# Kernel optimization log

Hardware: AMD Instinct MI355X
Metric: run time of the kernel (lower is better)

Reference implementation:

```python
import jax, jax.numpy as jnp
import numpy as np
from jax import lax

N, IN_CH, OUT_CH, KERNEL, D = 16, 256, 256, 3, 4096
FACTOR = 2  # upsampling factor
RESAMPLE_K = (1.0, 3.0, 3.0, 1.0)


def _fir_kernel():
    # _setup_kernel: normalize to sum 1; upsample path scales by gain * factor
    k = np.asarray(RESAMPLE_K, dtype=np.float32)
    k = k / k.sum()
    return k * FACTOR  # gain = 1


def setup_inputs() -> dict:
    key = jax.random.key(0)
    k1, k2, k3 = jax.random.split(key, 3)
    x = jax.random.normal(k1, (N, IN_CH, D), dtype=jnp.float32)
    weight = jax.random.normal(k2, (OUT_CH, IN_CH, KERNEL), dtype=jnp.float32) * 0.05
    bias = jax.random.normal(k3, (OUT_CH,), dtype=jnp.float32) * 0.05
    return {"x": x, "weight": weight, "bias": bias}


def _upfirdn1d(x, k, pad0, pad1):
    # up=down=1 path of StyleGAN2 upfirdn1d: pad, then TRUE convolution with FIR k
    # (torch native impl flips k before F.conv1d). Depthwise via [N*C,1,L] reshape.
    n, c, _ = x.shape
    xp = jnp.pad(x, ((0, 0), (0, 0), (pad0, pad1)))
    kr = k[::-1][None, None, :]  # flip -> correlation == convolution
    y = lax.conv_general_dilated(
        xp.reshape(n * c, 1, -1), kr, window_strides=(1,), padding=[(0, 0)],
        dimension_numbers=("NCH", "OIH", "NCH"))
    return y.reshape(n, c, -1)


def _upsample_conv_1d(x, w):
    # torch: w reshaped/flipped/permuted then conv_transpose1d(stride=factor).
    # conv_transpose with that transformed weight == correlation with the ORIGINAL
    # w on an input dilated by `factor` with (convH-1) padding on both sides
    # (output_padding = 0 for these shapes).
    convH = w.shape[2]
    y = lax.conv_general_dilated(
        x, w, window_strides=(1,), padding=[(convH - 1, convH - 1)],
        lhs_dilation=(FACTOR,), dimension_numbers=("NCH", "OIH", "NCH"))
    k = jnp.asarray(_fir_kernel())
    p = k.shape[0] - FACTOR - (convH - 1)  # = 0 here
    pad0 = (p + 1) // 2 + FACTOR - 1
    pad1 = p // 2 + 1
    return _upfirdn1d(y, k, pad0, pad1)  # -> [N, C_out, D * FACTOR]


def reference(x, weight, bias):
    y = _upsample_conv_1d(x, weight)
    return y + bias[None, :, None]
```

## Files before the change

kernel.cpp:

```cpp
#include <hip/hip_runtime.h>
#include <hip/hip_bf16.h>

#define N_   16
#define CI_  256
#define CO_  256
#define D_   4096
#define DO_  8192
#define KTOT 768
#define XTROWS 4098
#define WT_ELEMS (512 * KTOT)
#define XT_ELEMS ((size_t)N_ * XTROWS * 256)

typedef short frag8 __attribute__((ext_vector_type(8)));
typedef float facc4 __attribute__((ext_vector_type(4)));

static __device__ __forceinline__ unsigned short f2bf(float f) {
    union { __hip_bfloat16 h; unsigned short u; } cv;
    cv.h = __float2bfloat16(f);
    return cv.u;
}

static __device__ __forceinline__ unsigned int pack2(float lo, float hi) {
    return (unsigned int)f2bf(lo) | ((unsigned int)f2bf(hi) << 16);
}

static __device__ __forceinline__ void async16(unsigned short* lds, const unsigned short* g) {
    __builtin_amdgcn_global_load_lds(
        (const __attribute__((address_space(1))) unsigned int*)g,
        (__attribute__((address_space(3))) unsigned int*)lds, 16, 0, 0);
}

#define DSR_(dst, addr, litstr) \
    asm volatile("ds_read_b128 %0, %1 offset:" litstr : "=&v"(dst) : "v"(addr))

__global__ __launch_bounds__(256) void prep_wt(const float* __restrict__ w,
                                               unsigned short* __restrict__ Wt) {
    const int ci = threadIdx.x;
    const int co = blockIdx.x;
    const float* wp = w + ((size_t)co * CI_ + ci) * 3;
    const float w0 = wp[0], w1 = wp[1], w2 = wp[2];
    const float e0 = 0.25f * w1 + 0.75f * w0;
    const float e1 = 0.75f * w2 + 0.75f * w1 + 0.25f * w0;
    const float e2 = 0.25f * w2;
    const float o0 = 0.25f * w0;
    const float o1 = 0.25f * w2 + 0.75f * w1 + 0.75f * w0;
    const float o2 = 0.75f * w2 + 0.25f * w1;
    unsigned short* pe = Wt + (size_t)(co * 2 + 0) * KTOT;
    unsigned short* po = Wt + (size_t)(co * 2 + 1) * KTOT;
    pe[0 * 256 + ci] = f2bf(e0); pe[1 * 256 + ci] = f2bf(e1); pe[2 * 256 + ci] = f2bf(e2);
    po[0 * 256 + ci] = f2bf(o0); po[1 * 256 + ci] = f2bf(o1); po[2 * 256 + ci] = f2bf(o2);
}

__global__ __launch_bounds__(256) void prep_xt2(const float* __restrict__ x,
                                                unsigned short* __restrict__ xt) {
    __shared__ unsigned int Lp[32][133];
    const int tid = threadIdx.x;
    const int t0  = blockIdx.x * 32;
    const int n   = blockIdx.y;
    const float* xn = x + (size_t)n * CI_ * D_;
    unsigned short* slab = xt + (size_t)n * XTROWS * 256;

    if (t0 == 0 && tid < 128)       ((unsigned int*)slab)[tid] = 0u;
    if (t0 == D_ - 32 && tid < 128) ((unsigned int*)(slab + (size_t)(XTROWS - 1) * 256))[tid] = 0u;

    const int cp_l  = tid >> 3;
    const int t_off = (tid & 7) * 4;

    #pragma unroll
    for (int p = 0; p < 4; ++p) {
        const int ci0 = p * 64 + cp_l * 2;
        float4 a = *(const float4*)(xn + (size_t)ci0 * D_ + t0 + t_off);
        float4 b = *(const float4*)(xn + (size_t)(ci0 + 1) * D_ + t0 + t_off);
        const int cp = p * 32 + cp_l;
        Lp[t_off + 0][cp] = pack2(a.x, b.x);
        Lp[t_off + 1][cp] = pack2(a.y, b.y);
        Lp[t_off + 2][cp] = pack2(a.z, b.z);
        Lp[t_off + 3][cp] = pack2(a.w, b.w);
    }
    __syncthreads();

    #pragma unroll
    for (int it = 0; it < 4; ++it) {
        const int row = it * 8 + (tid >> 5);
        const int c4  = (tid & 31) * 4;
        uint4 v;
        v.x = Lp[row][c4 + 0];
        v.y = Lp[row][c4 + 1];
        v.z = Lp[row][c4 + 2];
        v.w = Lp[row][c4 + 3];
        *(uint4*)(slab + (size_t)(1 + t0 + row) * 256 + c4 * 2) = v;
    }
}

__global__ __launch_bounds__(512, 2) void gemm_upfir8(
    const unsigned short* __restrict__ Wt, const unsigned short* __restrict__ xt,
    const float* __restrict__ bias, float* __restrict__ out)
{
    __shared__ __align__(16) unsigned short SL[65536];

    const int tid  = threadIdx.x;
    const int lane = tid & 63;
    const int wid  = tid >> 6;
    const int quad = lane >> 4;
    const int l16  = lane & 15;

    const int bt0 = blockIdx.x * 256;
    const int bm0 = blockIdx.y * 256;
    const int n   = blockIdx.z;

    const int srow = wid * 16 + (lane >> 2);
    const int cg   = (lane & 3) ^ ((lane >> 3) & 3);
    const unsigned short* sA = Wt + (size_t)(bm0 + srow) * KTOT + cg * 8;
    const unsigned short* sB = xt + (size_t)n * XTROWS * 256
                                  + (size_t)(bt0 + srow) * 256 + cg * 8;

    #define STAGE_A(u, mh) do {                                                     \
        async16(SL + (((u)&1)*16384 + (mh)*8192 + 0*4096 + wid*512),                \
                sA + (size_t)(mh)*128*KTOT + (u)*64 + 0);                           \
        async16(SL + (((u)&1)*16384 + (mh)*8192 + 1*4096 + wid*512),                \
                sA + (size_t)(mh)*128*KTOT + (u)*64 + 32); } while (0)
    #define STAGE_B(u, th) do {                                                     \
        async16(SL + (32768 + ((u)&1)*16384 + (th)*8192 + 0*4096 + wid*512),        \
                sB + (size_t)(th)*128*256 + (u)*64 + 0);                            \
        async16(SL + (32768 + ((u)&1)*16384 + (th)*8192 + 1*4096 + wid*512),        \
                sB + (size_t)(th)*128*256 + (u)*64 + 32); } while (0)

    const int swz = quad ^ ((l16 >> 1) & 3);
    const int mh  = wid & 1;
    const int wm  = mh * 128;
    const int wt  = ((wid >> 1) & 3) * 64;
    const unsigned base = (unsigned)(size_t)&SL[0];
    const unsigned aB = base + (unsigned)(mh * 16384 + l16 * 64 + swz * 16);
    const unsigned bB = base + 65536u
                      + (unsigned)(((wid >> 2) & 1) * 16384
                                   + (((wid >> 1) & 1) * 64 + l16) * 64 + swz * 16);

    facc4 acc[8][4] = {};

    STAGE_A(0, 0); STAGE_A(0, 1); STAGE_B(0, 0); STAGE_B(0, 1);
    STAGE_A(1, 0); STAGE_A(1, 1);
    asm volatile("s_waitcnt vmcnt(4)" ::: "memory");
    __builtin_amdgcn_s_barrier();

    #define MM(m, t)                                                                 \
        acc[m][t] = __builtin_amdgcn_mfma_f32_16x16x32_bf16(a[m][0], b[t][0], acc[m][t], 0, 0, 0); \
        acc[m][t] = __builtin_amdgcn_mfma_f32_16x16x32_bf16(a[m][1], b[t][1], acc[m][t], 0, 0, 0);

    #pragma unroll 2
    for (int u = 0; u < 12; ++u) {
        const unsigned au = aB + (unsigned)((u & 1) << 15);
        const unsigned bu = bB + (unsigned)((u & 1) << 15);
        frag8 a[8][2], b[4][2];

        DSR_(a[0][0], au, "0");    DSR_(a[0][1], au, "8192");
        DSR_(a[1][0], au, "1024"); DSR_(a[1][1], au, "9216");
        DSR_(a[2][0], au, "2048"); DSR_(a[2][1], au, "10240");
        DSR_(a[3][0], au, "3072"); DSR_(a[3][1], au, "11264");
        DSR_(b[0][0], bu, "0");    DSR_(b[0][1], bu, "8192");
        DSR_(b[1][0], bu, "1024"); DSR_(b[1][1], bu, "9216");
        if (u < 11) STAGE_B(u + 1, 0);
        __builtin_amdgcn_s_barrier();
        asm volatile("s_waitcnt lgkmcnt(0)" ::: "memory");
        __builtin_amdgcn_sched_barrier(0);
        __builtin_amdgcn_s_setprio(1);
        MM(0, 0) MM(1, 0) MM(2, 0) MM(3, 0)
        MM(0, 1) MM(1, 1) MM(2, 1) MM(3, 1)
        __builtin_amdgcn_s_setprio(0);
        __builtin_amdgcn_s_barrier();

        DSR_(a[4][0], au, "4096"); DSR_(a[4][1], au, "12288");
        DSR_(a[5][0], au, "5120"); DSR_(a[5][1], au, "13312");
        DSR_(a[6][0], au, "6144"); DSR_(a[6][1], au, "14336");
        DSR_(a[7][0], au, "7168"); DSR_(a[7][1], au, "15360");
        if (u < 11) STAGE_B(u + 1, 1);
        __builtin_amdgcn_s_barrier();
        asm volatile("s_waitcnt lgkmcnt(0)" ::: "memory");
        __builtin_amdgcn_sched_barrier(0);
        __builtin_amdgcn_s_setprio(1);
        MM(4, 0) MM(5, 0) MM(6, 0) MM(7, 0)
        MM(4, 1) MM(5, 1) MM(6, 1) MM(7, 1)
        __builtin_amdgcn_s_setprio(0);
        __builtin_amdgcn_s_barrier();

        DSR_(b[2][0], bu, "2048"); DSR_(b[2][1], bu, "10240");
        DSR_(b[3][0], bu, "3072"); DSR_(b[3][1], bu, "11264");
        if (u < 10) STAGE_A(u + 2, 0);
        __builtin_amdgcn_s_barrier();
        asm volatile("s_waitcnt lgkmcnt(0)" ::: "memory");
        __builtin_amdgcn_sched_barrier(0);
        __builtin_amdgcn_s_setprio(1);
        MM(4, 2) MM(5, 2) MM(6, 2) MM(7, 2)
        MM(4, 3) MM(5, 3) MM(6, 3) MM(7, 3)
        __builtin_amdgcn_s_setprio(0);
        __builtin_amdgcn_s_barrier();

        if (u < 10) STAGE_A(u + 2, 1);
        __builtin_amdgcn_s_barrier();
        __builtin_amdgcn_sched_barrier(0);
        __builtin_amdgcn_s_setprio(1);
        MM(0, 2) MM(1, 2) MM(2, 2) MM(3, 2)
        MM(0, 3) MM(1, 3) MM(2, 3) MM(3, 3)
        __builtin_amdgcn_s_setprio(0);
        if (u < 10) { asm volatile("s_waitcnt vmcnt(4)" ::: "memory"); }
        else        { asm volatile("s_waitcnt vmcnt(0)" ::: "memory"); }
        __builtin_amdgcn_s_barrier();
    }
    #undef MM
    #undef STAGE_A
    #undef STAGE_B

    #pragma unroll
    for (int m8 = 0; m8 < 8; ++m8) {
        int m0  = bm0 + wm + m8 * 16 + quad * 4;
        int co0 = m0 >> 1;
        float b0 = bias[co0];
        float b1 = bias[co0 + 1];
        #pragma unroll
        for (int t4 = 0; t4 < 4; ++t4) {
            int t = bt0 + wt + t4 * 16 + l16;
            facc4 v = acc[m8][t4];
            float* p0 = out + ((size_t)(n * CO_ + co0)) * DO_ + 2 * t;
            float* p1 = p0 + DO_;
            *(float2*)p0 = make_float2(v.x + b0, v.y + b0);
            *(float2*)p1 = make_float2(v.z + b1, v.w + b1);
        }
    }
}

__global__ __launch_bounds__(256) void upconv_fir_f32(
    const float* __restrict__ x, const float* __restrict__ w,
    const float* __restrict__ bias, float* __restrict__ out)
{
    __shared__ float ws[CI_][4];
    const int tid = threadIdx.x;
    const int co  = blockIdx.y;
    const int n   = blockIdx.z;
    {
        const float* wc = w + (size_t)co * CI_ * 3;
        ws[tid][0] = wc[tid * 3 + 0];
        ws[tid][1] = wc[tid * 3 + 1];
        ws[tid][2] = wc[tid * 3 + 2];
        ws[tid][3] = 0.f;
    }
    __syncthreads();
    const int t0 = (blockIdx.x * 256 + tid) * 8;
    const float* xn = x + (size_t)n * CI_ * D_;
    float s[10], g[9];
    #pragma unroll
    for (int k = 0; k < 10; ++k) s[k] = 0.f;
    #pragma unroll
    for (int k = 0; k < 9; ++k) g[k] = 0.f;
    #pragma unroll 2
    for (int ci = 0; ci < CI_; ++ci) {
        const float* xr = xn + ci * D_;
        float4 va = *(const float4*)(xr + t0);
        float4 vb = *(const float4*)(xr + t0 + 4);
        float  xm = (t0 > 0)      ? xr[t0 - 1] : 0.f;
        float  xp = (t0 + 8 < D_) ? xr[t0 + 8] : 0.f;
        float4 wv = *(const float4*)(&ws[ci][0]);
        const float w0 = wv.x, w1 = wv.y, w2 = wv.z;
        float xa[10];
        xa[0] = xm; xa[1] = va.x; xa[2] = va.y; xa[3] = va.z; xa[4] = va.w;
        xa[5] = vb.x; xa[6] = vb.y; xa[7] = vb.z; xa[8] = vb.w; xa[9] = xp;
        #pragma unroll
        for (int k = 0; k < 10; ++k) s[k] += w1 * xa[k];
        #pragma unroll
        for (int k = 0; k < 9; ++k)  g[k] += w0 * xa[k] + w2 * xa[k + 1];
    }
    const float b = bias[co];
    float o16[16];
    #pragma unroll
    for (int tt = 0; tt < 8; ++tt) {
        o16[2 * tt]     = 0.25f * (s[tt] + g[tt + 1]) + 0.75f * (g[tt] + s[tt + 1]) + b;
        o16[2 * tt + 1] = 0.25f * (g[tt] + s[tt + 2]) + 0.75f * (s[tt + 1] + g[tt + 1]) + b;
    }
    float* ob = out + ((size_t)n * CO_ + co) * DO_ + 2 * t0;
    *(float4*)(ob + 0)  = make_float4(o16[0],  o16[1],  o16[2],  o16[3]);
    *(float4*)(ob + 4)  = make_float4(o16[4],  o16[5],  o16[6],  o16[7]);
    *(float4*)(ob + 8)  = make_float4(o16[8],  o16[9],  o16[10], o16[11]);
    *(float4*)(ob + 12) = make_float4(o16[12], o16[13], o16[14], o16[15]);
}

extern "C" void kernel_launch(void* const* d_in, const int* in_sizes, int n_in,
                              void* d_out, int out_size, void* d_ws, size_t ws_size,
                              hipStream_t stream) {
    const float* x  = (const float*)d_in[0];
    const float* w  = (const float*)d_in[1];
    const float* b  = (const float*)d_in[2];
    float* out      = (float*)d_out;

    const size_t need = (size_t)WT_ELEMS * 2 + XT_ELEMS * 2;
    if (ws_size >= need) {
        unsigned short* Wt = (unsigned short*)d_ws;
        unsigned short* xt = Wt + WT_ELEMS;
        prep_wt<<<dim3(CO_), 256, 0, stream>>>(w, Wt);
        prep_xt2<<<dim3(D_ / 32, N_), 256, 0, stream>>>(x, xt);
        gemm_upfir8<<<dim3(D_ / 256, 2, N_), 512, 0, stream>>>(Wt, xt, b, out);
    } else {
        upconv_fir_f32<<<dim3(2, CO_, N_), 256, 0, stream>>>(x, w, b, out);
    }
}
```

Baseline: 236.1 us.

## Fuse x transpose/bf16 conversion into GEMM and reuse halo'd B tile across taps

Removes the separate prep_xt2 pass that wrote a transposed bf16 copy of x to workspace. The GEMM now loads fp32 x directly, packs it to bf16 in registers and writes a swizzled LDS tile with one-row halos. It then reuses that single B tile for all three kernel taps by shifting the row offset, reordering K so each channel group covers three taps. This saves one kernel launch and a round trip of the activation tensor through global memory. In exchange the GEMM takes on register-staged global loads and more complex waitcnt scheduling inside the main loop.

Result: slower. 268.4 us (+13.7%).

```diff
diff --git a/kernel.cpp b/kernel.cpp
--- a/kernel.cpp
+++ b/kernel.cpp
@@ -7,9 +7,7 @@
 #define D_   4096
 #define DO_  8192
 #define KTOT 768
-#define XTROWS 4098
 #define WT_ELEMS (512 * KTOT)
-#define XT_ELEMS ((size_t)N_ * XTROWS * 256)
 
 typedef short frag8 __attribute__((ext_vector_type(8)));
 typedef float facc4 __attribute__((ext_vector_type(4)));
@@ -51,52 +49,11 @@
     po[0 * 256 + ci] = f2bf(o0); po[1 * 256 + ci] = f2bf(o1); po[2 * 256 + ci] = f2bf(o2);
 }
 
-__global__ __launch_bounds__(256) void prep_xt2(const float* __restrict__ x,
-                                                unsigned short* __restrict__ xt) {
-    __shared__ unsigned int Lp[32][133];
-    const int tid = threadIdx.x;
-    const int t0  = blockIdx.x * 32;
-    const int n   = blockIdx.y;
-    const float* xn = x + (size_t)n * CI_ * D_;
-    unsigned short* slab = xt + (size_t)n * XTROWS * 256;
-
-    if (t0 == 0 && tid < 128)       ((unsigned int*)slab)[tid] = 0u;
-    if (t0 == D_ - 32 && tid < 128) ((unsigned int*)(slab + (size_t)(XTROWS - 1) * 256))[tid] = 0u;
-
-    const int cp_l  = tid >> 3;
-    const int t_off = (tid & 7) * 4;
-
-    #pragma unroll
-    for (int p = 0; p < 4; ++p) {
-        const int ci0 = p * 64 + cp_l * 2;
-        float4 a = *(const float4*)(xn + (size_t)ci0 * D_ + t0 + t_off);
-        float4 b = *(const float4*)(xn + (size_t)(ci0 + 1) * D_ + t0 + t_off);
-        const int cp = p * 32 + cp_l;
-        Lp[t_off + 0][cp] = pack2(a.x, b.x);
-        Lp[t_off + 1][cp] = pack2(a.y, b.y);
-        Lp[t_off + 2][cp] = pack2(a.z, b.z);
-        Lp[t_off + 3][cp] = pack2(a.w, b.w);
-    }
-    __syncthreads();
-
-    #pragma unroll
-    for (int it = 0; it < 4; ++it) {
-        const int row = it * 8 + (tid >> 5);
-        const int c4  = (tid & 31) * 4;
-        uint4 v;
-        v.x = Lp[row][c4 + 0];
-        v.y = Lp[row][c4 + 1];
-        v.z = Lp[row][c4 + 2];
-        v.w = Lp[row][c4 + 3];
-        *(uint4*)(slab + (size_t)(1 + t0 + row) * 256 + c4 * 2) = v;
-    }
-}
-
-__global__ __launch_bounds__(512, 2) void gemm_upfir8(
-    const unsigned short* __restrict__ Wt, const unsigned short* __restrict__ xt,
+__global__ __launch_bounds__(512, 2) void gemm_fused(
+    const unsigned short* __restrict__ Wt, const float* __restrict__ x,
     const float* __restrict__ bias, float* __restrict__ out)
 {
-    __shared__ __align__(16) unsigned short SL[65536];
+    __shared__ __align__(16) unsigned short SL[49280];
 
     const int tid  = threadIdx.x;
     const int lane = tid & 63;
@@ -107,107 +64,146 @@
     const int bt0 = blockIdx.x * 256;
     const int bm0 = blockIdx.y * 256;
     const int n   = blockIdx.z;
+    const float* xn = x + (size_t)n * CI_ * D_;
 
     const int srow = wid * 16 + (lane >> 2);
     const int cg   = (lane & 3) ^ ((lane >> 3) & 3);
     const unsigned short* sA = Wt + (size_t)(bm0 + srow) * KTOT + cg * 8;
-    const unsigned short* sB = xt + (size_t)n * XTROWS * 256
-                                  + (size_t)(bt0 + srow) * 256 + cg * 8;
-
-    #define STAGE_A(u, mh) do {                                                     \
-        async16(SL + (((u)&1)*16384 + (mh)*8192 + 0*4096 + wid*512),                \
-                sA + (size_t)(mh)*128*KTOT + (u)*64 + 0);                           \
-        async16(SL + (((u)&1)*16384 + (mh)*8192 + 1*4096 + wid*512),                \
-                sA + (size_t)(mh)*128*KTOT + (u)*64 + 32); } while (0)
-    #define STAGE_B(u, th) do {                                                     \
-        async16(SL + (32768 + ((u)&1)*16384 + (th)*8192 + 0*4096 + wid*512),        \
-                sB + (size_t)(th)*128*256 + (u)*64 + 0);                            \
-        async16(SL + (32768 + ((u)&1)*16384 + (th)*8192 + 1*4096 + wid*512),        \
-                sB + (size_t)(th)*128*256 + (u)*64 + 32); } while (0)
+
+    const int cp = tid >> 4;
+    const int tq = tid & 15;
 
     const int swz = quad ^ ((l16 >> 1) & 3);
     const int mh  = wid & 1;
     const int wm  = mh * 128;
     const int wt  = ((wid >> 1) & 3) * 64;
     const unsigned base = (unsigned)(size_t)&SL[0];
-    const unsigned aB = base + (unsigned)(mh * 16384 + l16 * 64 + swz * 16);
-    const unsigned bB = base + 65536u
-                      + (unsigned)(((wid >> 2) & 1) * 16384
-                                   + (((wid >> 1) & 1) * 64 + l16) * 64 + swz * 16);
+    const unsigned aB  = base + (unsigned)(mh * 16384 + l16 * 64 + swz * 16);
+    const unsigned bxb = base + 65536u;
 
     facc4 acc[8][4] = {};
 
-    STAGE_A(0, 0); STAGE_A(0, 1); STAGE_B(0, 0); STAGE_B(0, 1);
-    STAGE_A(1, 0); STAGE_A(1, 1);
+    const int KOFF[14] = {0,256,512, 64,320,576, 128,384,640, 192,448,704, 704,704};
+
+    #define STAGE_A(kt2, koff) do { const int par_ = (kt2) & 1;                     \
+        async16(SL + par_*16384 + 0*8192 + 0*4096 + wid*512, sA + (size_t)0*128*KTOT + (koff) + 0);  \
+        async16(SL + par_*16384 + 0*8192 + 1*4096 + wid*512, sA + (size_t)0*128*KTOT + (koff) + 32); \
+        async16(SL + par_*16384 + 1*8192 + 0*4096 + wid*512, sA + (size_t)1*128*KTOT + (koff) + 0);  \
+        async16(SL + par_*16384 + 1*8192 + 1*4096 + wid*512, sA + (size_t)1*128*KTOT + (koff) + 32); \
+    } while (0)
+
+    float4 va[4], vb[4];
+    float  h0 = 0.f, h1 = 0.f;
+    #define BLOAD(g2) do {                                                          \
+        const float* bsrc = xn + (size_t)((g2)*64 + cp*2) * D_ + bt0;               \
+        _Pragma("unroll") for (int s_ = 0; s_ < 4; ++s_) {                          \
+            va[s_] = *(const float4*)(bsrc + s_*64 + tq*4);                         \
+            vb[s_] = *(const float4*)(bsrc + D_ + s_*64 + tq*4); }                  \
+        { int cph = tid & 31; int hrow = (tid & 32) ? 257 : 0;                      \
+          int th  = bt0 - 1 + hrow;                                                 \
+          int tcl = th < 0 ? 0 : (th > D_-1 ? D_-1 : th);                           \
+          const float* hsrc = xn + (size_t)((g2)*64 + cph*2) * D_ + tcl;            \
+          h0 = hsrc[0]; h1 = hsrc[D_]; }                                            \
+    } while (0)
+
+    #define BWRITE() do {                                                           \
+        _Pragma("unroll") for (int s_ = 0; s_ < 4; ++s_)                            \
+        _Pragma("unroll") for (int e_ = 0; e_ < 4; ++e_) {                          \
+            int row = s_*64 + tq*4 + 1 + e_;                                        \
+            unsigned pc = (((unsigned)(cp >> 2) ^ (unsigned)(row & 7)) << 2) | (unsigned)(cp & 3); \
+            *(unsigned*)((char*)SL + 65536u + (unsigned)row*128u + pc*4u) =         \
+                pack2(((const float*)&va[s_])[e_], ((const float*)&vb[s_])[e_]); }  \
+        if (tid < 64) {                                                             \
+            int cph = tid & 31; int hrow = (tid & 32) ? 257 : 0;                    \
+            int th  = bt0 - 1 + hrow;                                               \
+            int ok  = (th >= 0) && (th < D_);                                       \
+            unsigned pc = (((unsigned)(cph >> 2) ^ (unsigned)(hrow & 7)) << 2) | (unsigned)(cph & 3); \
+            *(unsigned*)((char*)SL + 65536u + (unsigned)hrow*128u + pc*4u) =        \
+                ok ? pack2(h0, h1) : 0u; }                                          \
+    } while (0)
+
+    #define MM_(M, T, AF)                                                                        \
+        acc[M][T] = __builtin_amdgcn_mfma_f32_16x16x32_bf16(AF[0], b[T][0], acc[M][T], 0, 0, 0); \
+        acc[M][T] = __builtin_amdgcn_mfma_f32_16x16x32_bf16(AF[1], b[T][1], acc[M][T], 0, 0, 0);
+
+    #define PHASE_SYNC() do {                                        \
+        asm volatile("s_waitcnt lgkmcnt(0)" ::: "memory");           \
+        __builtin_amdgcn_sched_barrier(0);                           \
+        __builtin_amdgcn_s_barrier();                                \
+        __builtin_amdgcn_sched_barrier(0);                           \
+    } while (0)
+
+    BLOAD(0);
+    asm volatile("" ::: "memory");
+    STAGE_A(0, KOFF[0]);
+    STAGE_A(1, KOFF[1]);
+    asm volatile("s_waitcnt vmcnt(8)" ::: "memory");
+    BWRITE();
     asm volatile("s_waitcnt vmcnt(4)" ::: "memory");
-    __builtin_amdgcn_s_barrier();
-
-    #define MM(m, t)                                                                 \
-        acc[m][t] = __builtin_amdgcn_mfma_f32_16x16x32_bf16(a[m][0], b[t][0], acc[m][t], 0, 0, 0); \
-        acc[m][t] = __builtin_amdgcn_mfma_f32_16x16x32_bf16(a[m][1], b[t][1], acc[m][t], 0, 0, 0);
-
-    #pragma unroll 2
-    for (int u = 0; u < 12; ++u) {
-        const unsigned au = aB + (unsigned)((u & 1) << 15);
-        const unsigned bu = bB + (unsigned)((u & 1) << 15);
-        frag8 a[8][2], b[4][2];
-
-        DSR_(a[0][0], au, "0");    DSR_(a[0][1], au, "8192");
-        DSR_(a[1][0], au, "1024"); DSR_(a[1][1], au, "9216");
-        DSR_(a[2][0], au, "2048"); DSR_(a[2][1], au, "10240");
-        DSR_(a[3][0], au, "3072"); DSR_(a[3][1], au, "11264");
-        DSR_(b[0][0], bu, "0");    DSR_(b[0][1], bu, "8192");
-        DSR_(b[1][0], bu, "1024"); DSR_(b[1][1], bu, "9216");
-        if (u < 11) STAGE_B(u + 1, 0);
-        __builtin_amdgcn_s_barrier();
-        asm volatile("s_waitcnt lgkmcnt(0)" ::: "memory");
-        __builtin_amdgcn_sched_barrier(0);
-        __builtin_amdgcn_s_setprio(1);
-        MM(0, 0) MM(1, 0) MM(2, 0) MM(3, 0)
-        MM(0, 1) MM(1, 1) MM(2, 1) MM(3, 1)
-        __builtin_amdgcn_s_setprio(0);
-        __builtin_amdgcn_s_barrier();
-
-        DSR_(a[4][0], au, "4096"); DSR_(a[4][1], au, "12288");
-        DSR_(a[5][0], au, "5120"); DSR_(a[5][1], au, "13312");
-        DSR_(a[6][0], au, "6144"); DSR_(a[6][1], au, "14336");
-        DSR_(a[7][0], au, "7168"); DSR_(a[7][1], au, "15360");
-        if (u < 11) STAGE_B(u + 1, 1);
-        __builtin_amdgcn_s_barrier();
-        asm volatile("s_waitcnt lgkmcnt(0)" ::: "memory");
-        __builtin_amdgcn_sched_barrier(0);
-        __builtin_amdgcn_s_setprio(1);
-        MM(4, 0) MM(5, 0) MM(6, 0) MM(7, 0)
-        MM(4, 1) MM(5, 1) MM(6, 1) MM(7, 1)
-        __builtin_amdgcn_s_setprio(0);
-        __builtin_amdgcn_s_barrier();
-
-        DSR_(b[2][0], bu, "2048"); DSR_(b[2][1], bu, "10240");
-        DSR_(b[3][0], bu, "3072"); DSR_(b[3][1], bu, "11264");
-        if (u < 10) STAGE_A(u + 2, 0);
-        __builtin_amdgcn_s_barrier();
-        asm volatile("s_waitcnt lgkmcnt(0)" ::: "memory");
-        __builtin_amdgcn_sched_barrier(0);
-        __builtin_amdgcn_s_setprio(1);
-        MM(4, 2) MM(5, 2) MM(6, 2) MM(7, 2)
-        MM(4, 3) MM(5, 3) MM(6, 3) MM(7, 3)
-        __builtin_amdgcn_s_setprio(0);
-        __builtin_amdgcn_s_barrier();
-
-        if (u < 10) STAGE_A(u + 2, 1);
-        __builtin_amdgcn_s_barrier();
-        __builtin_amdgcn_sched_barrier(0);
-        __builtin_amdgcn_s_setprio(1);
-        MM(0, 2) MM(1, 2) MM(2, 2) MM(3, 2)
-        MM(0, 3) MM(1, 3) MM(2, 3) MM(3, 3)
-        __builtin_amdgcn_s_setprio(0);
-        if (u < 10) { asm volatile("s_waitcnt vmcnt(4)" ::: "memory"); }
-        else        { asm volatile("s_waitcnt vmcnt(0)" ::: "memory"); }
-        __builtin_amdgcn_s_barrier();
-    }
-    #undef MM
+    PHASE_SYNC();
+
+    #pragma unroll
+    for (int kt = 0; kt < 12; ++kt) {
+        const int j = kt % 3;
+        const unsigned au = aB + (unsigned)((kt & 1) * 32768);
+        const int rowc = wt + l16 + j;
+        const unsigned rb = bxb + (unsigned)rowc * 128u;
+        const unsigned bk0 = rb + (unsigned)(((quad    ) ^ (rowc & 7)) << 4);
+        const unsigned bk1 = rb + (unsigned)(((quad + 4) ^ (rowc & 7)) << 4);
+
+        frag8 aLo[4][2], aHi[4][2], b[4][2];
+
+        DSR_(aLo[0][0], au, "0");    DSR_(aLo[0][1], au, "8192");
+        DSR_(aLo[1][0], au, "1024"); DSR_(aLo[1][1], au, "9216");
+        DSR_(aLo[2][0], au, "2048"); DSR_(aLo[2][1], au, "10240");
+        DSR_(aLo[3][0], au, "3072"); DSR_(aLo[3][1], au, "11264");
+        DSR_(b[0][0], bk0, "0");     DSR_(b[0][1], bk1, "0");
+        DSR_(b[1][0], bk0, "2048");  DSR_(b[1][1], bk1, "2048");
+        PHASE_SYNC();
+        __builtin_amdgcn_s_setprio(1);
+        MM_(0,0,aLo[0]) MM_(1,0,aLo[1]) MM_(2,0,aLo[2]) MM_(3,0,aLo[3])
+        MM_(0,1,aLo[0]) MM_(1,1,aLo[1]) MM_(2,1,aLo[2]) MM_(3,1,aLo[3])
+        __builtin_amdgcn_s_setprio(0);
+
+        DSR_(b[2][0], bk0, "4096");  DSR_(b[2][1], bk1, "4096");
+        DSR_(b[3][0], bk0, "6144");  DSR_(b[3][1], bk1, "6144");
+        PHASE_SYNC();
+        __builtin_amdgcn_s_setprio(1);
+        MM_(0,2,aLo[0]) MM_(1,2,aLo[1]) MM_(2,2,aLo[2]) MM_(3,2,aLo[3])
+        MM_(0,3,aLo[0]) MM_(1,3,aLo[1]) MM_(2,3,aLo[2]) MM_(3,3,aLo[3])
+        __builtin_amdgcn_s_setprio(0);
+
+        DSR_(aHi[0][0], au, "4096"); DSR_(aHi[0][1], au, "12288");
+        DSR_(aHi[1][0], au, "5120"); DSR_(aHi[1][1], au, "13312");
+        DSR_(aHi[2][0], au, "6144"); DSR_(aHi[2][1], au, "14336");
+        DSR_(aHi[3][0], au, "7168"); DSR_(aHi[3][1], au, "15360");
+        PHASE_SYNC();
+        __builtin_amdgcn_s_setprio(1);
+        MM_(4,0,aHi[0]) MM_(5,0,aHi[1]) MM_(6,0,aHi[2]) MM_(7,0,aHi[3])
+        MM_(4,1,aHi[0]) MM_(5,1,aHi[1]) MM_(6,1,aHi[2]) MM_(7,1,aHi[3])
+        __builtin_amdgcn_s_setprio(0);
+
+        if (j == 2) {
+            asm volatile("s_waitcnt vmcnt(4)" ::: "memory");
+            BWRITE();
+        }
+        STAGE_A(kt + 2, KOFF[kt + 2]);
+        if (j == 0) BLOAD(((kt / 3) + 1) & 3);
+        if (j == 2) { asm volatile("s_waitcnt vmcnt(4)"  ::: "memory"); }
+        else        { asm volatile("s_waitcnt vmcnt(14)" ::: "memory"); }
+        PHASE_SYNC();
+        __builtin_amdgcn_s_setprio(1);
+        MM_(4,2,aHi[0]) MM_(5,2,aHi[1]) MM_(6,2,aHi[2]) MM_(7,2,aHi[3])
+        MM_(4,3,aHi[0]) MM_(5,3,aHi[1]) MM_(6,3,aHi[2]) MM_(7,3,aHi[3])
+        __builtin_amdgcn_s_setprio(0);
+    }
+    asm volatile("s_waitcnt vmcnt(0)" ::: "memory");
+
+    #undef MM_
+    #undef PHASE_SYNC
     #undef STAGE_A
-    #undef STAGE_B
+    #undef BLOAD
+    #undef BWRITE
 
     #pragma unroll
     for (int m8 = 0; m8 < 8; ++m8) {
@@ -289,13 +285,11 @@
     const float* b  = (const float*)d_in[2];
     float* out      = (float*)d_out;
 
-    const size_t need = (size_t)WT_ELEMS * 2 + XT_ELEMS * 2;
+    const size_t need = (size_t)WT_ELEMS * 2;
     if (ws_size >= need) {
         unsigned short* Wt = (unsigned short*)d_ws;
-        unsigned short* xt = Wt + WT_ELEMS;
         prep_wt<<<dim3(CO_), 256, 0, stream>>>(w, Wt);
-        prep_xt2<<<dim3(D_ / 32, N_), 256, 0, stream>>>(x, xt);
-        gemm_upfir8<<<dim3(D_ / 256, 2, N_), 512, 0, stream>>>(Wt, xt, b, out);
+        gemm_fused<<<dim3(D_ / 256, 2, N_), 512, 0, stream>>>(Wt, x, b, out);
     } else {
         upconv_fir_f32<<<dim3(2, CO_, N_), 256, 0, stream>>>(x, w, b, out);
     }
```
